# Kernel tuning notes

Hardware: AMD Instinct MI355X
Metric: run time of the kernel (lower is better)

The kernel has to match this reference:

```python
import jax, jax.numpy as jnp
import numpy as np

B_SZ, SEQ, H, P, N, LBLK = 16, 2048, 16, 64, 16, 64  # batch, seqlen, heads, d_head, d_state, block_len


def setup_inputs() -> dict:
    key = jax.random.key(0)
    k1, k2, k3, k4 = jax.random.split(key, 4)
    X = jax.random.normal(k1, (B_SZ, SEQ, H, P), jnp.float32)
    # A is a per-step log-decay; real Mamba2 has A < 0 so exp(segsum) stays bounded
    A = -0.1 * jax.random.uniform(k2, (B_SZ, SEQ, H), jnp.float32)
    B = jax.random.normal(k3, (B_SZ, SEQ, H, N), jnp.float32)
    C = jax.random.normal(k4, (B_SZ, SEQ, H, N), jnp.float32)
    return {"X": X, "A": A, "B": B, "C": C}


def _exp_segsum(x):
    """x: (..., t). Returns exp(cumsum[i]-cumsum[j]) for j<=i, 0 above diagonal."""
    t = x.shape[-1]
    cs = jnp.cumsum(x, axis=-1)
    diff = cs[..., :, None] - cs[..., None, :]
    mask = jnp.tril(jnp.ones((t, t), dtype=bool))
    return jnp.where(mask, jnp.exp(jnp.where(mask, diff, 0.0)), 0.0)


def ssd_forward(X, A, B, C):
    b, s, h, p = X.shape
    n = B.shape[-1]
    c = s // LBLK
    # chunk: (b, c, l, h, *)
    Xb = X.reshape(b, c, LBLK, h, p)
    Bb = B.reshape(b, c, LBLK, h, n)
    Cb = C.reshape(b, c, LBLK, h, n)
    Ab = jnp.transpose(A.reshape(b, c, LBLK, h), (0, 3, 1, 2))  # (b, h, c, l)
    A_cs = jnp.cumsum(Ab, axis=-1)                               # (b, h, c, l)

    # 1. intra-chunk (diagonal block) output: kernel 1
    L = _exp_segsum(Ab)                                          # (b, h, c, l, s)
    CB = jnp.einsum("bclhn,bcshn->bhcls", Cb, Bb)               # (b, h, c, l, s)
    Y_diag = jnp.einsum("bhcls,bcshp->bclhp", CB * L, Xb)

    # 2. per-chunk end states: kernel 2
    decay_states = jnp.exp(A_cs[..., -1:] - A_cs)                # (b, h, c, l)
    states = jnp.einsum("bclhn,bhcl,bclhp->bchpn", Bb, decay_states, Xb)

    # 3. inter-chunk recurrence (zero initial state): kernel 3
    states = jnp.concatenate([jnp.zeros_like(states[:, :1]), states], axis=1)  # (b, c+1, h, p, n)
    A_last_pad = jnp.pad(A_cs[..., -1], ((0, 0), (0, 0), (1, 0)))              # (b, h, c+1)
    decay_chunk = _exp_segsum(A_last_pad)                                       # (b, h, c+1, c+1)
    new_states = jnp.einsum("bhzc,bchpn->bzhpn", decay_chunk, states)
    states_in = new_states[:, :-1]                                              # (b, c, h, p, n)

    # 4. off-diagonal (state -> output) contribution: kernel 4
    Y_off = jnp.einsum("bclhn,bchpn,bhcl->bclhp", Cb, states_in, jnp.exp(A_cs))

    return (Y_diag + Y_off).reshape(b, s, h, p)


def reference(X, A, B, C):
    return ssd_forward(X, A, B, C)
```

## Files before the change

### kernel.cpp

```cpp
#include <hip/hip_runtime.h>

#define BS 16
#define SEQL 2048
#define NH 16
#define PD 64
#define ND 16
#define LB 64
#define NC 32
#define NHP (NH * PD)
#define NHN (NH * ND)

typedef __attribute__((ext_vector_type(8))) short bf16x8;
typedef __attribute__((ext_vector_type(4))) float f32x4;

static __device__ __forceinline__ unsigned short f2bf(float x) {
  unsigned int u = __float_as_uint(x);
  return (unsigned short)((u + 0x7FFFu + ((u >> 16) & 1u)) >> 16);
}
static __device__ __forceinline__ unsigned int pk2(float a, float b) {
  return (unsigned int)f2bf(a) | ((unsigned int)f2bf(b) << 16);
}

static __device__ __forceinline__ void barrier_lds() {
  __builtin_amdgcn_sched_barrier(0);
  asm volatile("s_waitcnt lgkmcnt(0)" ::: "memory");
  __builtin_amdgcn_s_barrier();
  __builtin_amdgcn_sched_barrier(0);
}

static __device__ __forceinline__ int invperm(int l) {
  const int jp = l >> 5, v = l & 31;
  return jp * 32 + (v < 16 ? (((v >> 2) << 3) | (v & 3))
                           : ((((v - 16) >> 2) << 3) | 4 | ((v - 16) & 3)));
}

__global__ __launch_bounds__(512) void ssd_fused(
    const float* __restrict__ Xg, const float* __restrict__ Ag,
    const float* __restrict__ Bg, const float* __restrict__ Cg,
    float* __restrict__ Yg) {
  const int h = blockIdx.x & (NH - 1);
  const int b = blockIdx.x >> 4;
  const int t = threadIdx.x;
  const int w = t >> 6;
  const int lane = t & 63;
  const int g = lane >> 4;
  const int cc = lane & 15;

  __shared__ __align__(16) unsigned short sXt[PD][64];
  __shared__ __align__(16) unsigned short sB[LB][ND + 8];
  __shared__ __align__(16) unsigned short sC[LB][ND + 8];
  __shared__ __align__(16) unsigned short sBdT[ND][LB + 8];
  __shared__ __align__(16) float sSTf[2][PD][ND + 4];
  __shared__ __align__(16) unsigned short sSTb[2][PD][ND + 8];
  __shared__ float sER[NC][LB];
  __shared__ float sRR[NC][LB];
  __shared__ float sEtot[NC];

  {
    float av[4];
#pragma unroll
    for (int k = 0; k < 4; ++k)
      av[k] = Ag[((size_t)(b * SEQL + (w + 8 * k) * LB + lane)) * NH + h];
#pragma unroll
    for (int k = 0; k < 4; ++k) {
      const int c = w + 8 * k;
      float v = av[k];
#pragma unroll
      for (int d = 1; d < 64; d <<= 1) {
        float o = __shfl_up(v, d, 64);
        if (lane >= d) v += o;
      }
      const float e = expf(v);
      sER[c][lane] = e;
      sRR[c][lane] = expf(-v);
      if (lane == 63) sEtot[c] = e;
    }
  }
  for (int i = t; i < PD * (ND + 4); i += 512) ((float*)sSTf[0])[i] = 0.f;
  for (int i = t; i < PD * (ND + 8); i += 512) ((unsigned short*)sSTb[0])[i] = 0;

  const int xl0 = (t >> 4) * 2, xp0 = (t & 15) * 4;
  const int bl = t >> 3, bn0 = (t & 7) * 2;
  const int mX = invperm(xl0);
  const int mB = invperm(bl);
  float4 px0, px1;
  float2 pb2, pc2;

#define PREF(ci) do { \
    const size_t s0_ = (size_t)(b * SEQL + (ci) * LB); \
    px0 = *(const float4*)&Xg[(s0_ + xl0) * NHP + h * PD + xp0]; \
    px1 = *(const float4*)&Xg[(s0_ + xl0 + 1) * NHP + h * PD + xp0]; \
    pb2 = *(const float2*)&Bg[(s0_ + bl) * NHN + h * ND + bn0]; \
    pc2 = *(const float2*)&Cg[(s0_ + bl) * NHN + h * ND + bn0]; \
  } while (0)

  const bf16x8 zf8 = {0, 0, 0, 0, 0, 0, 0, 0};
  auto xfrag = [&](int p_, int kb) -> bf16x8 {
    return *(const bf16x8*)&sXt[p_][(kb ^ ((p_ >> 3) & 7)) << 3];
  };

  PREF(0);
  __syncthreads();

  for (int c = 0; c < NC; ++c) {
    {
#pragma unroll
      for (int j = 0; j < 4; ++j) {
        const int p_ = xp0 + j;
        const int mm = ((((mX >> 3) ^ ((p_ >> 3) & 7)) << 3) | (mX & 7));
        *(unsigned int*)&sXt[p_][mm] = pk2((&px0.x)[j], (&px1.x)[j]);
      }
      const float el = sER[c][bl];
      const float dl = sEtot[c] * sRR[c][bl];
      *(unsigned int*)&sB[bl][bn0] = pk2(pb2.x, pb2.y);
      *(unsigned int*)&sC[bl][bn0] = pk2(el * pc2.x, el * pc2.y);
      sBdT[bn0][mB] = f2bf(dl * pb2.x);
      sBdT[bn0 + 1][mB] = f2bf(dl * pb2.y);
    }
    if (c + 1 < NC) PREF(c + 1);
    barrier_lds();

    const int cur = c & 1, nxt = cur ^ 1;
    if (w < 4) {
      const int lb = w;
      const int l = lb * 16 + cc;
      bf16x8 cf = zf8;
      if (g < 2) cf = *(const bf16x8*)&sC[l][g * 8];
      auto mtile = [&](int sb, bool mask) -> uint2 {
        bf16x8 bfr = zf8;
        if (g < 2) bfr = *(const bf16x8*)&sB[sb * 16 + cc][g * 8];
        f32x4 z4 = {0.f, 0.f, 0.f, 0.f};
        f32x4 d = __builtin_amdgcn_mfma_f32_16x16x32_bf16(bfr, cf, z4, 0, 0, 0);
        float m[4];
#pragma unroll
        for (int r = 0; r < 4; ++r) {
          m[r] = d[r] * sRR[c][sb * 16 + 4 * g + r];
          if (mask && (4 * g + r) > cc) m[r] = 0.f;
        }
        return make_uint2(pk2(m[0], m[1]), pk2(m[2], m[3]));
      };
      union {
        bf16x8 v;
        unsigned int u[4];
      } mf0, mf1;
      mf0.u[0] = mf0.u[1] = mf0.u[2] = mf0.u[3] = 0u;
      mf1.u[0] = mf1.u[1] = mf1.u[2] = mf1.u[3] = 0u;
      if (lb == 0) {
        const uint2 t0 = mtile(0, true);
        mf0.u[0] = t0.x; mf0.u[1] = t0.y;
      } else if (lb == 1) {
        const uint2 t0 = mtile(0, false), t1 = mtile(1, true);
        mf0.u[0] = t0.x; mf0.u[1] = t0.y; mf0.u[2] = t1.x; mf0.u[3] = t1.y;
      } else if (lb == 2) {
        const uint2 t0 = mtile(0, false), t1 = mtile(1, false), t2 = mtile(2, true);
        mf0.u[0] = t0.x; mf0.u[1] = t0.y; mf0.u[2] = t1.x; mf0.u[3] = t1.y;
        mf1.u[0] = t2.x; mf1.u[1] = t2.y;
      } else {
        const uint2 t0 = mtile(0, false), t1 = mtile(1, false);
        const uint2 t2 = mtile(2, false), t3 = mtile(3, true);
        mf0.u[0] = t0.x; mf0.u[1] = t0.y; mf0.u[2] = t1.x; mf0.u[3] = t1.y;
        mf1.u[0] = t2.x; mf1.u[1] = t2.y; mf1.u[2] = t3.x; mf1.u[3] = t3.y;
      }
#pragma unroll
      for (int pb = 0; pb < 4; ++pb) {
        const int p = pb * 16 + cc;
        bf16x8 stf = zf8;
        if (g < 2) stf = *(const bf16x8*)&sSTb[cur][p][g * 8];
        f32x4 acc = {0.f, 0.f, 0.f, 0.f};
        acc = __builtin_amdgcn_mfma_f32_16x16x32_bf16(cf, stf, acc, 0, 0, 0);
        acc = __builtin_amdgcn_mfma_f32_16x16x32_bf16(mf0.v, xfrag(p, g), acc, 0, 0, 0);
        if (lb >= 2)
          acc = __builtin_amdgcn_mfma_f32_16x16x32_bf16(mf1.v, xfrag(p, 4 + g), acc, 0, 0, 0);
        const size_t yb =
            ((size_t)(b * SEQL + c * LB + lb * 16 + 4 * g)) * NHP + h * PD + p;
#pragma unroll
        for (int r = 0; r < 4; ++r) Yg[yb + (size_t)r * NHP] = acc[r];
      }
    } else {
      const int pS = (w - 4) * 16 + cc;
      bf16x8 ad0 = *(const bf16x8*)&sBdT[cc][g * 8];
      bf16x8 ad1 = *(const bf16x8*)&sBdT[cc][32 + g * 8];
      f32x4 s4 = {0.f, 0.f, 0.f, 0.f};
      s4 = __builtin_amdgcn_mfma_f32_16x16x32_bf16(ad0, xfrag(pS, g), s4, 0, 0, 0);
      s4 = __builtin_amdgcn_mfma_f32_16x16x32_bf16(ad1, xfrag(pS, 4 + g), s4, 0, 0, 0);
      const float etot = sEtot[c];
      float4 old = *(const float4*)&sSTf[cur][pS][4 * g];
      float4 nw;
      nw.x = old.x * etot + s4[0];
      nw.y = old.y * etot + s4[1];
      nw.z = old.z * etot + s4[2];
      nw.w = old.w * etot + s4[3];
      *(float4*)&sSTf[nxt][pS][4 * g] = nw;
      uint2 ub;
      ub.x = pk2(nw.x, nw.y);
      ub.y = pk2(nw.z, nw.w);
      *(uint2*)&sSTb[nxt][pS][4 * g] = ub;
    }
    barrier_lds();
  }
#undef PREF
}

extern "C" void kernel_launch(void* const* d_in, const int* in_sizes, int n_in,
                              void* d_out, int out_size, void* d_ws, size_t ws_size,
                              hipStream_t stream) {
  (void)in_sizes; (void)n_in; (void)out_size; (void)d_ws; (void)ws_size;
  const float* X = (const float*)d_in[0];
  const float* A = (const float*)d_in[1];
  const float* B = (const float*)d_in[2];
  const float* C = (const float*)d_in[3];
  float* Y = (float*)d_out;
  ssd_fused<<<BS * NH, 512, 0, stream>>>(X, A, B, C, Y);
}
```

Baseline: 76.42 us.

## Double-buffer chunk staging in LDS and rebalance output work across all warps

The per-chunk X/B/C staging buffers are double-buffered, so chunk c+1 is written to shared memory during chunk c's compute. This removes one of the two block-wide barriers per chunk, and global prefetch now runs two chunks ahead. Output work is split so all 8 warps compute Y (each handles half of the p-blocks), and the first 4 warps also do the state update. The cost is duplicated CB-matrix computation across warp pairs and more LDS use.

```diff
diff --git a/kernel.cpp b/kernel.cpp
--- a/kernel.cpp
+++ b/kernel.cpp
@@ -46,10 +46,10 @@
   const int g = lane >> 4;
   const int cc = lane & 15;
 
-  __shared__ __align__(16) unsigned short sXt[PD][64];
-  __shared__ __align__(16) unsigned short sB[LB][ND + 8];
-  __shared__ __align__(16) unsigned short sC[LB][ND + 8];
-  __shared__ __align__(16) unsigned short sBdT[ND][LB + 8];
+  __shared__ __align__(16) unsigned short sXt[2][PD][64];
+  __shared__ __align__(16) unsigned short sB[2][LB][ND + 8];
+  __shared__ __align__(16) unsigned short sC[2][LB][ND + 8];
+  __shared__ __align__(16) unsigned short sBdT[2][ND][LB + 8];
   __shared__ __align__(16) float sSTf[2][PD][ND + 4];
   __shared__ __align__(16) unsigned short sSTb[2][PD][ND + 8];
   __shared__ float sER[NC][LB];
@@ -94,111 +94,118 @@
     pc2 = *(const float2*)&Cg[(s0_ + bl) * NHN + h * ND + bn0]; \
   } while (0)
 
+#define STAGE(bufi, ci) do { \
+    _Pragma("unroll") \
+    for (int j_ = 0; j_ < 4; ++j_) { \
+      const int p_ = xp0 + j_; \
+      const int mm_ = ((((mX >> 3) ^ ((p_ >> 3) & 7)) << 3) | (mX & 7)); \
+      *(unsigned int*)&sXt[bufi][p_][mm_] = pk2((&px0.x)[j_], (&px1.x)[j_]); \
+    } \
+    { const float el_ = sER[ci][bl]; \
+      const float dl_ = sEtot[ci] * sRR[ci][bl]; \
+      *(unsigned int*)&sB[bufi][bl][bn0] = pk2(pb2.x, pb2.y); \
+      *(unsigned int*)&sC[bufi][bl][bn0] = pk2(el_ * pc2.x, el_ * pc2.y); \
+      sBdT[bufi][bn0][mB] = f2bf(dl_ * pb2.x); \
+      sBdT[bufi][bn0 + 1][mB] = f2bf(dl_ * pb2.y); } \
+  } while (0)
+
   const bf16x8 zf8 = {0, 0, 0, 0, 0, 0, 0, 0};
-  auto xfrag = [&](int p_, int kb) -> bf16x8 {
-    return *(const bf16x8*)&sXt[p_][(kb ^ ((p_ >> 3) & 7)) << 3];
+  auto xfrag = [&](int buf, int p_, int kb) -> bf16x8 {
+    return *(const bf16x8*)&sXt[buf][p_][(kb ^ ((p_ >> 3) & 7)) << 3];
   };
 
   PREF(0);
-  __syncthreads();
+  STAGE(0, 0);
+  PREF(1);
+  barrier_lds();
+
+  const int lb = w >> 1;
+  const int pb0 = (w & 1) * 2;
+  const int l = lb * 16 + cc;
 
   for (int c = 0; c < NC; ++c) {
-    {
-#pragma unroll
-      for (int j = 0; j < 4; ++j) {
-        const int p_ = xp0 + j;
-        const int mm = ((((mX >> 3) ^ ((p_ >> 3) & 7)) << 3) | (mX & 7));
-        *(unsigned int*)&sXt[p_][mm] = pk2((&px0.x)[j], (&px1.x)[j]);
+    const int db = c & 1, nb = db ^ 1;
+
+    bf16x8 cf = zf8;
+    if (g < 2) cf = *(const bf16x8*)&sC[db][l][g * 8];
+    auto mtile = [&](int sb, bool mask) -> uint2 {
+      bf16x8 bfr = zf8;
+      if (g < 2) bfr = *(const bf16x8*)&sB[db][sb * 16 + cc][g * 8];
+      f32x4 z4 = {0.f, 0.f, 0.f, 0.f};
+      f32x4 d = __builtin_amdgcn_mfma_f32_16x16x32_bf16(bfr, cf, z4, 0, 0, 0);
+      float m[4];
+#pragma unroll
+      for (int r = 0; r < 4; ++r) {
+        m[r] = d[r] * sRR[c][sb * 16 + 4 * g + r];
+        if (mask && (4 * g + r) > cc) m[r] = 0.f;
       }
-      const float el = sER[c][bl];
-      const float dl = sEtot[c] * sRR[c][bl];
-      *(unsigned int*)&sB[bl][bn0] = pk2(pb2.x, pb2.y);
-      *(unsigned int*)&sC[bl][bn0] = pk2(el * pc2.x, el * pc2.y);
-      sBdT[bn0][mB] = f2bf(dl * pb2.x);
-      sBdT[bn0 + 1][mB] = f2bf(dl * pb2.y);
-    }
-    if (c + 1 < NC) PREF(c + 1);
-    barrier_lds();
-
-    const int cur = c & 1, nxt = cur ^ 1;
+      return make_uint2(pk2(m[0], m[1]), pk2(m[2], m[3]));
+    };
+    union { bf16x8 v; unsigned int u[4]; } mf0, mf1;
+    mf0.u[0] = mf0.u[1] = mf0.u[2] = mf0.u[3] = 0u;
+    mf1.u[0] = mf1.u[1] = mf1.u[2] = mf1.u[3] = 0u;
+    if (lb == 0) {
+      const uint2 t0 = mtile(0, true);
+      mf0.u[0] = t0.x; mf0.u[1] = t0.y;
+    } else if (lb == 1) {
+      const uint2 t0 = mtile(0, false), t1 = mtile(1, true);
+      mf0.u[0] = t0.x; mf0.u[1] = t0.y; mf0.u[2] = t1.x; mf0.u[3] = t1.y;
+    } else if (lb == 2) {
+      const uint2 t0 = mtile(0, false), t1 = mtile(1, false), t2 = mtile(2, true);
+      mf0.u[0] = t0.x; mf0.u[1] = t0.y; mf0.u[2] = t1.x; mf0.u[3] = t1.y;
+      mf1.u[0] = t2.x; mf1.u[1] = t2.y;
+    } else {
+      const uint2 t0 = mtile(0, false), t1 = mtile(1, false);
+      const uint2 t2 = mtile(2, false), t3 = mtile(3, true);
+      mf0.u[0] = t0.x; mf0.u[1] = t0.y; mf0.u[2] = t1.x; mf0.u[3] = t1.y;
+      mf1.u[0] = t2.x; mf1.u[1] = t2.y; mf1.u[2] = t3.x; mf1.u[3] = t3.y;
+    }
+
+#pragma unroll
+    for (int pbi = 0; pbi < 2; ++pbi) {
+      const int p = (pb0 + pbi) * 16 + cc;
+      bf16x8 stf = zf8;
+      if (g < 2) stf = *(const bf16x8*)&sSTb[db][p][g * 8];
+      f32x4 acc = {0.f, 0.f, 0.f, 0.f};
+      acc = __builtin_amdgcn_mfma_f32_16x16x32_bf16(cf, stf, acc, 0, 0, 0);
+      acc = __builtin_amdgcn_mfma_f32_16x16x32_bf16(mf0.v, xfrag(db, p, g), acc, 0, 0, 0);
+      if (lb >= 2)
+        acc = __builtin_amdgcn_mfma_f32_16x16x32_bf16(mf1.v, xfrag(db, p, 4 + g), acc, 0, 0, 0);
+      const size_t yb =
+          ((size_t)(b * SEQL + c * LB + lb * 16 + 4 * g)) * NHP + h * PD + p;
+#pragma unroll
+      for (int r = 0; r < 4; ++r) Yg[yb + (size_t)r * NHP] = acc[r];
+    }
+
     if (w < 4) {
-      const int lb = w;
-      const int l = lb * 16 + cc;
-      bf16x8 cf = zf8;
-      if (g < 2) cf = *(const bf16x8*)&sC[l][g * 8];
-      auto mtile = [&](int sb, bool mask) -> uint2 {
-        bf16x8 bfr = zf8;
-        if (g < 2) bfr = *(const bf16x8*)&sB[sb * 16 + cc][g * 8];
-        f32x4 z4 = {0.f, 0.f, 0.f, 0.f};
-        f32x4 d = __builtin_amdgcn_mfma_f32_16x16x32_bf16(bfr, cf, z4, 0, 0, 0);
-        float m[4];
-#pragma unroll
-        for (int r = 0; r < 4; ++r) {
-          m[r] = d[r] * sRR[c][sb * 16 + 4 * g + r];
-          if (mask && (4 * g + r) > cc) m[r] = 0.f;
-        }
-        return make_uint2(pk2(m[0], m[1]), pk2(m[2], m[3]));
-      };
-      union {
-        bf16x8 v;
-        unsigned int u[4];
-      } mf0, mf1;
-      mf0.u[0] = mf0.u[1] = mf0.u[2] = mf0.u[3] = 0u;
-      mf1.u[0] = mf1.u[1] = mf1.u[2] = mf1.u[3] = 0u;
-      if (lb == 0) {
-        const uint2 t0 = mtile(0, true);
-        mf0.u[0] = t0.x; mf0.u[1] = t0.y;
-      } else if (lb == 1) {
-        const uint2 t0 = mtile(0, false), t1 = mtile(1, true);
-        mf0.u[0] = t0.x; mf0.u[1] = t0.y; mf0.u[2] = t1.x; mf0.u[3] = t1.y;
-      } else if (lb == 2) {
-        const uint2 t0 = mtile(0, false), t1 = mtile(1, false), t2 = mtile(2, true);
-        mf0.u[0] = t0.x; mf0.u[1] = t0.y; mf0.u[2] = t1.x; mf0.u[3] = t1.y;
-        mf1.u[0] = t2.x; mf1.u[1] = t2.y;
-      } else {
-        const uint2 t0 = mtile(0, false), t1 = mtile(1, false);
-        const uint2 t2 = mtile(2, false), t3 = mtile(3, true);
-        mf0.u[0] = t0.x; mf0.u[1] = t0.y; mf0.u[2] = t1.x; mf0.u[3] = t1.y;
-        mf1.u[0] = t2.x; mf1.u[1] = t2.y; mf1.u[2] = t3.x; mf1.u[3] = t3.y;
-      }
-#pragma unroll
-      for (int pb = 0; pb < 4; ++pb) {
-        const int p = pb * 16 + cc;
-        bf16x8 stf = zf8;
-        if (g < 2) stf = *(const bf16x8*)&sSTb[cur][p][g * 8];
-        f32x4 acc = {0.f, 0.f, 0.f, 0.f};
-        acc = __builtin_amdgcn_mfma_f32_16x16x32_bf16(cf, stf, acc, 0, 0, 0);
-        acc = __builtin_amdgcn_mfma_f32_16x16x32_bf16(mf0.v, xfrag(p, g), acc, 0, 0, 0);
-        if (lb >= 2)
-          acc = __builtin_amdgcn_mfma_f32_16x16x32_bf16(mf1.v, xfrag(p, 4 + g), acc, 0, 0, 0);
-        const size_t yb =
-            ((size_t)(b * SEQL + c * LB + lb * 16 + 4 * g)) * NHP + h * PD + p;
-#pragma unroll
-        for (int r = 0; r < 4; ++r) Yg[yb + (size_t)r * NHP] = acc[r];
-      }
-    } else {
-      const int pS = (w - 4) * 16 + cc;
-      bf16x8 ad0 = *(const bf16x8*)&sBdT[cc][g * 8];
-      bf16x8 ad1 = *(const bf16x8*)&sBdT[cc][32 + g * 8];
+      const int pS = w * 16 + cc;
+      bf16x8 ad0 = *(const bf16x8*)&sBdT[db][cc][g * 8];
+      bf16x8 ad1 = *(const bf16x8*)&sBdT[db][cc][32 + g * 8];
       f32x4 s4 = {0.f, 0.f, 0.f, 0.f};
-      s4 = __builtin_amdgcn_mfma_f32_16x16x32_bf16(ad0, xfrag(pS, g), s4, 0, 0, 0);
-      s4 = __builtin_amdgcn_mfma_f32_16x16x32_bf16(ad1, xfrag(pS, 4 + g), s4, 0, 0, 0);
+      s4 = __builtin_amdgcn_mfma_f32_16x16x32_bf16(ad0, xfrag(db, pS, g), s4, 0, 0, 0);
+      s4 = __builtin_amdgcn_mfma_f32_16x16x32_bf16(ad1, xfrag(db, pS, 4 + g), s4, 0, 0, 0);
       const float etot = sEtot[c];
-      float4 old = *(const float4*)&sSTf[cur][pS][4 * g];
+      float4 old = *(const float4*)&sSTf[db][pS][4 * g];
       float4 nw;
       nw.x = old.x * etot + s4[0];
       nw.y = old.y * etot + s4[1];
       nw.z = old.z * etot + s4[2];
       nw.w = old.w * etot + s4[3];
-      *(float4*)&sSTf[nxt][pS][4 * g] = nw;
+      *(float4*)&sSTf[nb][pS][4 * g] = nw;
       uint2 ub;
       ub.x = pk2(nw.x, nw.y);
       ub.y = pk2(nw.z, nw.w);
-      *(uint2*)&sSTb[nxt][pS][4 * g] = ub;
+      *(uint2*)&sSTb[nb][pS][4 * g] = ub;
+    }
+
+    if (c + 1 < NC) {
+      STAGE(nb, c + 1);
+      if (c + 2 < NC) PREF(c + 2);
     }
     barrier_lds();
   }
 #undef PREF
+#undef STAGE
 }
 
 extern "C" void kernel_launch(void* const* d_in, const int* in_sizes, int n_in,
```

After: 75.57 us. No clear change (-1.1%).
